# Kernel tuning notes

Hardware: AMD Instinct MI355X
Metric: run time of the kernel (lower is better)

Reference implementation:

```python
import jax, jax.numpy as jnp
import numpy as np

# db4 (Daubechies-4) lowpass decomposition filter, L = 8 taps
DB4 = np.array([0.23037781330885523, 0.7148465705525415, 0.6308807679295904,
                -0.027983769416983849, -0.18703481171888114, 0.030841381835986965,
                0.032883011666982945, -0.010597401784997278], dtype=np.float32)


def setup_inputs() -> dict:
    key = jax.random.key(0)
    x = jax.random.normal(key, (4, 256, 256, 256), dtype=jnp.float32)
    h = jnp.asarray(DB4)
    return {"x": x, "h": h}


def _corr_valid(u, f):
    # u: [..., T], f: [L]; cross-correlation with VALID padding (== tf.nn.conv1d)
    L = f.shape[0]
    B = int(np.prod(u.shape[:-1]))
    out = jax.lax.conv_general_dilated(
        u.reshape(B, 1, u.shape[-1]), f.reshape(1, 1, L),
        window_strides=(1,), padding='VALID',
        dimension_numbers=('NCW', 'OIW', 'NCW'))
    return out.reshape(u.shape[:-1] + (out.shape[-1],))


def _recon_axis(s, w, h0, h1, axis):
    # s, w: scale / wavelet coefficient halves, same shape; recon along `axis`
    L = h0.shape[0]
    P = (L - 2) // 2 + 1  # number of periodic-wrap samples (= L//2 for even L)
    x = jnp.stack([s, w])                      # [2, ...]
    x = jnp.moveaxis(x, axis + 1, -1)          # bring recon axis to last
    N = x.shape[-1]
    # periodic extension (cyclic gather of last P) then drop first -> len N+P-1
    x = jnp.concatenate([x[..., N - P:], x], axis=-1)[..., 1:]
    # zero-interleaved upsample: [0, x0, 0, x1, ...], then one trailing zero -> len 2N+L-1
    up = jnp.stack([jnp.zeros_like(x), x], axis=-1).reshape(x.shape[:-1] + (-1,))
    up = jnp.pad(up, [(0, 0)] * (up.ndim - 1) + [(0, 1)])
    y = _corr_valid(up[0], h0) + _corr_valid(up[1], h1)  # [..., 2N]
    return jnp.moveaxis(y, -1, axis)


def reference(x, h):
    h0 = h[::-1]                                        # reversed lowpass
    sign = jnp.where(jnp.arange(h.shape[0]) % 2 == 0, -1.0, 1.0).astype(h.dtype)
    h1 = sign * h                                       # QMF highpass (double reverse cancels)
    out = x
    for axis in range(1, x.ndim):
        s, w = jnp.split(out, 2, axis=axis)
        out = _recon_axis(s, w, h0, h1, axis)
    return out
```

## Files before the change

### kernel.cpp

```cpp
#include <hip/hip_runtime.h>


typedef float f32x2 __attribute__((ext_vector_type(2)));

#define FILT_DECL(h)                                          \
  const float a0 = h[6], a1 = h[4], a2 = h[2], a3 = h[0];     \
  const float b0 = h[7], b1 = h[5], b2 = h[3], b3 = h[1];     \
  const float c0 = h[1], c1 = h[3], c2 = h[5], c3 = h[7];     \
  const float d0 = -h[0], d1 = -h[2], d2 = -h[4], d3 = -h[6];

#define Y0(s0,s1,s2,s3,w0,w1,w2,w3)                                        \
  fmaf(w3, c3, fmaf(w2, c2, fmaf(w1, c1, fmaf(w0, c0,                      \
  fmaf(s3, a3, fmaf(s2, a2, fmaf(s1, a1, s0 * a0)))))))
#define Y1(s0,s1,s2,s3,w0,w1,w2,w3)                                        \
  fmaf(w3, d3, fmaf(w2, d2, fmaf(w1, d1, fmaf(w0, d0,                      \
  fmaf(s3, b3, fmaf(s2, b2, fmaf(s1, b1, s0 * b0)))))))

#define PKFMA(s, k, acc) __builtin_elementwise_fma((f32x2){(s),(s)}, (k), (acc))

__device__ __forceinline__ void gload_lds4(const float* g, float* l) {
  auto gp = reinterpret_cast<const __attribute__((address_space(1))) int*>(
      reinterpret_cast<uintptr_t>(g));
  auto lp = reinterpret_cast<__attribute__((address_space(3))) int*>(
      reinterpret_cast<uintptr_t>(l));
  __builtin_amdgcn_global_load_lds(gp, lp, 4, 0, 0);
}

__global__ __launch_bounds__(256) void wav_axis1_s(const float* __restrict__ in,
                                                   float* __restrict__ tmp,
                                                   const float* __restrict__ h) {
  const int inner = blockIdx.x * 256 + threadIdx.x;
  const int m0 = blockIdx.y * 64;
  const size_t base = (size_t)blockIdx.z * (256u * 65536u) + (unsigned)inner;
  const float* __restrict__ ps = in + base;
  const float* __restrict__ pw = in + base + (size_t)128 * 65536;
  float* __restrict__ po = tmp + base;
  FILT_DECL(h)
  float s0 = __builtin_nontemporal_load(&ps[(size_t)((m0 - 3) & 127) * 65536]);
  float s1 = __builtin_nontemporal_load(&ps[(size_t)((m0 - 2) & 127) * 65536]);
  float s2 = __builtin_nontemporal_load(&ps[(size_t)((m0 - 1) & 127) * 65536]);
  float w0 = __builtin_nontemporal_load(&pw[(size_t)((m0 - 3) & 127) * 65536]);
  float w1 = __builtin_nontemporal_load(&pw[(size_t)((m0 - 2) & 127) * 65536]);
  float w2 = __builtin_nontemporal_load(&pw[(size_t)((m0 - 1) & 127) * 65536]);
  for (int m = m0; m < m0 + 64; ++m) {
    const float s3 = __builtin_nontemporal_load(&ps[(size_t)m * 65536]);
    const float w3 = __builtin_nontemporal_load(&pw[(size_t)m * 65536]);
    po[(size_t)(2 * m) * 65536] = Y0(s0, s1, s2, s3, w0, w1, w2, w3);
    po[(size_t)(2 * m + 1) * 65536] = Y1(s0, s1, s2, s3, w0, w1, w2, w3);
    s0 = s1; s1 = s2; s2 = s3;
    w0 = w1; w1 = w2; w2 = w3;
  }
}

#define LSTR 264
__global__ __launch_bounds__(256, 7) void wav_t23s(const float* __restrict__ tmp,
                                                   float* __restrict__ out,
                                                   const float* __restrict__ hg) {
  __shared__ __align__(16) float lb[22 * LSTR];
  const int t = threadIdx.x;
  const int d2t = blockIdx.x;
  const size_t slice = blockIdx.y;
  const float* __restrict__ src = tmp + slice * 65536;
  FILT_DECL(hg)
  const f32x2 AB0 = {a0, b0}, AB1 = {a1, b1}, AB2 = {a2, b2}, AB3 = {a3, b3};
  const f32x2 CD0 = {c0, d0}, CD1 = {c1, d1}, CD2 = {c2, d2}, CD3 = {c3, d3};
  const int mb2 = 8 * d2t - 3;

  {
    const int phys = t + ((t < 128) ? 3 : 7);
#pragma unroll
    for (int k = 0; k < 11; ++k) {
      const int g2 = (mb2 + k) & 127;
      gload_lds4(src + (g2 << 8) + t, &lb[k * LSTR + phys]);
    }
#pragma unroll
    for (int k = 0; k < 11; ++k) {
      const int g2 = 128 + ((mb2 + k) & 127);
      gload_lds4(src + (g2 << 8) + t, &lb[(11 + k) * LSTR + phys]);
    }
  }
  __syncthreads();

  {
    const int pj = t + ((t < 128) ? 3 : 7);
    float S[11], W[11];
#pragma unroll
    for (int i = 0; i < 11; ++i) S[i] = lb[i * LSTR + pj];
#pragma unroll
    for (int i = 0; i < 11; ++i) W[i] = lb[(11 + i) * LSTR + pj];
    const int hcol = (t >= 125 && t < 128) ? (t - 125)
                   : ((t >= 253) ? (t - 121) : -1);
#pragma unroll
    for (int q = 0; q < 8; ++q) {
      f32x2 acc = (f32x2){S[q], S[q]} * AB0;
      acc = PKFMA(S[q+1], AB1, acc);
      acc = PKFMA(S[q+2], AB2, acc);
      acc = PKFMA(S[q+3], AB3, acc);
      acc = PKFMA(W[q],   CD0, acc);
      acc = PKFMA(W[q+1], CD1, acc);
      acc = PKFMA(W[q+2], CD2, acc);
      acc = PKFMA(W[q+3], CD3, acc);
      lb[q * LSTR + pj] = acc.x;
      lb[(11 + q) * LSTR + pj] = acc.y;
      if (hcol >= 0) {
        lb[q * LSTR + hcol] = acc.x;
        lb[(11 + q) * LSTR + hcol] = acc.y;
      }
    }
  }
  __syncthreads();

  const int r = t >> 4, m0 = (t & 15) * 8;
  const int prow = ((r & 1) ? (11 + (r >> 1)) : (r >> 1)) * LSTR;
  float S[11], W[11];
  {
    const float4 sa = *reinterpret_cast<const float4*>(&lb[prow + m0]);
    const float4 sb = *reinterpret_cast<const float4*>(&lb[prow + m0 + 4]);
    const float2 sc = *reinterpret_cast<const float2*>(&lb[prow + m0 + 8]);
    S[0]=sa.x; S[1]=sa.y; S[2]=sa.z; S[3]=sa.w;
    S[4]=sb.x; S[5]=sb.y; S[6]=sb.z; S[7]=sb.w;
    S[8]=sc.x; S[9]=sc.y; S[10]=lb[prow + m0 + 10];
    const float4 wa = *reinterpret_cast<const float4*>(&lb[prow + 132 + m0]);
    const float4 wb = *reinterpret_cast<const float4*>(&lb[prow + 132 + m0 + 4]);
    const float2 wc = *reinterpret_cast<const float2*>(&lb[prow + 132 + m0 + 8]);
    W[0]=wa.x; W[1]=wa.y; W[2]=wa.z; W[3]=wa.w;
    W[4]=wb.x; W[5]=wb.y; W[6]=wb.z; W[7]=wb.w;
    W[8]=wc.x; W[9]=wc.y; W[10]=lb[prow + 132 + m0 + 10];
  }
  float* __restrict__ dst = out + slice * 65536
      + (size_t)(16 * d2t + r) * 256 + 16 * (t & 15);
#pragma unroll
  for (int g = 0; g < 4; ++g) {
    f32x2 eA = (f32x2){S[2*g], S[2*g]} * AB0;
    eA = PKFMA(S[2*g+1], AB1, eA);
    eA = PKFMA(S[2*g+2], AB2, eA);
    eA = PKFMA(S[2*g+3], AB3, eA);
    eA = PKFMA(W[2*g],   CD0, eA);
    eA = PKFMA(W[2*g+1], CD1, eA);
    eA = PKFMA(W[2*g+2], CD2, eA);
    eA = PKFMA(W[2*g+3], CD3, eA);
    f32x2 eB = (f32x2){S[2*g+1], S[2*g+1]} * AB0;
    eB = PKFMA(S[2*g+2], AB1, eB);
    eB = PKFMA(S[2*g+3], AB2, eB);
    eB = PKFMA(S[2*g+4], AB3, eB);
    eB = PKFMA(W[2*g+1], CD0, eB);
    eB = PKFMA(W[2*g+2], CD1, eB);
    eB = PKFMA(W[2*g+3], CD2, eB);
    eB = PKFMA(W[2*g+4], CD3, eB);
    *reinterpret_cast<float4*>(dst + 4 * g) = make_float4(eA.x, eA.y, eB.x, eB.y);
  }
}

__global__ __launch_bounds__(256) void wav_axis1(const float* __restrict__ in,
                                                 float* __restrict__ out,
                                                 const float* __restrict__ h) {
  const int inner = blockIdx.x * 256 + threadIdx.x;
  const int m0 = blockIdx.y * 64;
  const size_t base = (size_t)blockIdx.z * (256u * 65536u) + (unsigned)inner;
  const float* __restrict__ ps = in + base;
  const float* __restrict__ pw = in + base + (size_t)128 * 65536;
  float* __restrict__ po = out + base;
  FILT_DECL(h)
  float s0 = ps[(size_t)((m0 - 3) & 127) * 65536];
  float s1 = ps[(size_t)((m0 - 2) & 127) * 65536];
  float s2 = ps[(size_t)((m0 - 1) & 127) * 65536];
  float w0 = pw[(size_t)((m0 - 3) & 127) * 65536];
  float w1 = pw[(size_t)((m0 - 2) & 127) * 65536];
  float w2 = pw[(size_t)((m0 - 1) & 127) * 65536];
  for (int m = m0; m < m0 + 64; ++m) {
    const float s3 = ps[(size_t)m * 65536];
    const float w3 = pw[(size_t)m * 65536];
    po[(size_t)(2 * m) * 65536] = Y0(s0, s1, s2, s3, w0, w1, w2, w3);
    po[(size_t)(2 * m + 1) * 65536] = Y1(s0, s1, s2, s3, w0, w1, w2, w3);
    s0 = s1; s1 = s2; s2 = s3;
    w0 = w1; w1 = w2; w2 = w3;
  }
}

__global__ __launch_bounds__(256) void wav_axis2(float* __restrict__ buf,
                                                 const float* __restrict__ h) {
  __shared__ float tile[256][32];
  const int t = threadIdx.x;
  const int c = t & 31;
  const int g = t >> 5;
  const size_t slice = (size_t)(blockIdx.x >> 3);
  const int col0 = (blockIdx.x & 7) * 32;
  float* __restrict__ p = buf + slice * 65536 + col0;
#pragma unroll
  for (int i = 0; i < 32; ++i) {
    const int rr = i * 8 + g;
    tile[rr][c] = p[rr * 256 + c];
  }
  __syncthreads();
  FILT_DECL(h)
  const int m0 = g * 16;
  float s0 = tile[(m0 - 3) & 127][c];
  float s1 = tile[(m0 - 2) & 127][c];
  float s2 = tile[(m0 - 1) & 127][c];
  float w0 = tile[128 + ((m0 - 3) & 127)][c];
  float w1 = tile[128 + ((m0 - 2) & 127)][c];
  float w2 = tile[128 + ((m0 - 1) & 127)][c];
#pragma unroll
  for (int m = m0; m < m0 + 16; ++m) {
    const float s3 = tile[m][c];
    const float w3 = tile[128 + m][c];
    p[(2 * m) * 256 + c] = Y0(s0, s1, s2, s3, w0, w1, w2, w3);
    p[(2 * m + 1) * 256 + c] = Y1(s0, s1, s2, s3, w0, w1, w2, w3);
    s0 = s1; s1 = s2; s2 = s3;
    w0 = w1; w1 = w2; w2 = w3;
  }
}

__global__ __launch_bounds__(256) void wav_axis3(float* __restrict__ buf,
                                                 const float* __restrict__ h) {
  __shared__ float tile[512];
  const int t = threadIdx.x;
  float* __restrict__ p = buf + (size_t)blockIdx.x * 512;
  tile[t] = p[t];
  tile[256 + t] = p[256 + t];
  __syncthreads();
  FILT_DECL(h)
  const int rr = t >> 7;
  const int m = t & 127;
  const float* __restrict__ line = tile + rr * 256;
  const float s0 = line[(m - 3) & 127];
  const float s1 = line[(m - 2) & 127];
  const float s2 = line[(m - 1) & 127];
  const float s3 = line[m];
  const float w0 = line[128 + ((m - 3) & 127)];
  const float w1 = line[128 + ((m - 2) & 127)];
  const float w2 = line[128 + ((m - 1) & 127)];
  const float w3 = line[128 + m];
  float2 y;
  y.x = Y0(s0, s1, s2, s3, w0, w1, w2, w3);
  y.y = Y1(s0, s1, s2, s3, w0, w1, w2, w3);
  *reinterpret_cast<float2*>(p + rr * 256 + 2 * m) = y;
}

extern "C" void kernel_launch(void* const* d_in, const int* in_sizes, int n_in,
                              void* d_out, int out_size, void* d_ws, size_t ws_size,
                              hipStream_t stream) {
  const float* x = (const float*)d_in[0];
  const float* h = (const float*)d_in[1];
  float* out = (float*)d_out;
  const size_t need = (size_t)4 * 256 * 256 * 256 * 4;

  if (ws_size >= need) {
    float* tmp = (float*)d_ws;
    wav_axis1_s<<<dim3(256, 2, 4), 256, 0, stream>>>(x, tmp, h);
    wav_t23s<<<dim3(16, 1024), 256, 0, stream>>>(tmp, out, h);
  } else {
    wav_axis1<<<dim3(256, 2, 4), 256, 0, stream>>>(x, out, h);
    wav_axis2<<<dim3(8192), 256, 0, stream>>>(out, h);
    wav_axis3<<<dim3(131072), 256, 0, stream>>>(out, h);
  }
}
```

Measured before the change: 220.6 us.

## Make second-stage kernel persistent per slice with double-buffered LDS prefetch

The fused axis-2/3 kernel now launches one block per 256x256 slice instead of one block per 16-row tile. Each block walks all 16 tiles in a loop, and the async global-to-LDS loads for the next tile go into a second LDS buffer while the current tile is computed. The aim is to hide global load latency behind compute and cut per-block launch and setup cost. In exchange the grid shrinks to 1024 blocks, per-block LDS usage doubles and the occupancy hint is dropped, so fewer waves may be resident per CU to hide memory latency.

```diff
diff --git a/kernel.cpp b/kernel.cpp
--- a/kernel.cpp
+++ b/kernel.cpp
@@ -53,101 +53,113 @@
 }
 
 #define LSTR 264
-__global__ __launch_bounds__(256, 7) void wav_t23s(const float* __restrict__ tmp,
-                                                   float* __restrict__ out,
-                                                   const float* __restrict__ hg) {
-  __shared__ __align__(16) float lb[22 * LSTR];
+__global__ __launch_bounds__(256) void wav_t23p(const float* __restrict__ tmp,
+                                                float* __restrict__ out,
+                                                const float* __restrict__ hg) {
+  __shared__ __align__(16) float lb[2][22 * LSTR];
   const int t = threadIdx.x;
-  const int d2t = blockIdx.x;
-  const size_t slice = blockIdx.y;
+  const size_t slice = blockIdx.x;
   const float* __restrict__ src = tmp + slice * 65536;
+  float* __restrict__ dstb = out + slice * 65536 + 16 * (t & 15);
   FILT_DECL(hg)
   const f32x2 AB0 = {a0, b0}, AB1 = {a1, b1}, AB2 = {a2, b2}, AB3 = {a3, b3};
   const f32x2 CD0 = {c0, d0}, CD1 = {c1, d1}, CD2 = {c2, d2}, CD3 = {c3, d3};
-  const int mb2 = 8 * d2t - 3;
-
-  {
-    const int phys = t + ((t < 128) ? 3 : 7);
-#pragma unroll
-    for (int k = 0; k < 11; ++k) {
-      const int g2 = (mb2 + k) & 127;
-      gload_lds4(src + (g2 << 8) + t, &lb[k * LSTR + phys]);
-    }
-#pragma unroll
-    for (int k = 0; k < 11; ++k) {
-      const int g2 = 128 + ((mb2 + k) & 127);
-      gload_lds4(src + (g2 << 8) + t, &lb[(11 + k) * LSTR + phys]);
-    }
-  }
-  __syncthreads();
-
-  {
-    const int pj = t + ((t < 128) ? 3 : 7);
-    float S[11], W[11];
-#pragma unroll
-    for (int i = 0; i < 11; ++i) S[i] = lb[i * LSTR + pj];
-#pragma unroll
-    for (int i = 0; i < 11; ++i) W[i] = lb[(11 + i) * LSTR + pj];
-    const int hcol = (t >= 125 && t < 128) ? (t - 125)
-                   : ((t >= 253) ? (t - 121) : -1);
-#pragma unroll
-    for (int q = 0; q < 8; ++q) {
-      f32x2 acc = (f32x2){S[q], S[q]} * AB0;
-      acc = PKFMA(S[q+1], AB1, acc);
-      acc = PKFMA(S[q+2], AB2, acc);
-      acc = PKFMA(S[q+3], AB3, acc);
-      acc = PKFMA(W[q],   CD0, acc);
-      acc = PKFMA(W[q+1], CD1, acc);
-      acc = PKFMA(W[q+2], CD2, acc);
-      acc = PKFMA(W[q+3], CD3, acc);
-      lb[q * LSTR + pj] = acc.x;
-      lb[(11 + q) * LSTR + pj] = acc.y;
-      if (hcol >= 0) {
-        lb[q * LSTR + hcol] = acc.x;
-        lb[(11 + q) * LSTR + hcol] = acc.y;
-      }
-    }
-  }
-  __syncthreads();
-
+  const int phys = t + ((t < 128) ? 3 : 7);
+  const int hcol = (t >= 125 && t < 128) ? (t - 125)
+                 : ((t >= 253) ? (t - 121) : -1);
   const int r = t >> 4, m0 = (t & 15) * 8;
   const int prow = ((r & 1) ? (11 + (r >> 1)) : (r >> 1)) * LSTR;
-  float S[11], W[11];
+
   {
-    const float4 sa = *reinterpret_cast<const float4*>(&lb[prow + m0]);
-    const float4 sb = *reinterpret_cast<const float4*>(&lb[prow + m0 + 4]);
-    const float2 sc = *reinterpret_cast<const float2*>(&lb[prow + m0 + 8]);
-    S[0]=sa.x; S[1]=sa.y; S[2]=sa.z; S[3]=sa.w;
-    S[4]=sb.x; S[5]=sb.y; S[6]=sb.z; S[7]=sb.w;
-    S[8]=sc.x; S[9]=sc.y; S[10]=lb[prow + m0 + 10];
-    const float4 wa = *reinterpret_cast<const float4*>(&lb[prow + 132 + m0]);
-    const float4 wb = *reinterpret_cast<const float4*>(&lb[prow + 132 + m0 + 4]);
-    const float2 wc = *reinterpret_cast<const float2*>(&lb[prow + 132 + m0 + 8]);
-    W[0]=wa.x; W[1]=wa.y; W[2]=wa.z; W[3]=wa.w;
-    W[4]=wb.x; W[5]=wb.y; W[6]=wb.z; W[7]=wb.w;
-    W[8]=wc.x; W[9]=wc.y; W[10]=lb[prow + 132 + m0 + 10];
-  }
-  float* __restrict__ dst = out + slice * 65536
-      + (size_t)(16 * d2t + r) * 256 + 16 * (t & 15);
-#pragma unroll
-  for (int g = 0; g < 4; ++g) {
-    f32x2 eA = (f32x2){S[2*g], S[2*g]} * AB0;
-    eA = PKFMA(S[2*g+1], AB1, eA);
-    eA = PKFMA(S[2*g+2], AB2, eA);
-    eA = PKFMA(S[2*g+3], AB3, eA);
-    eA = PKFMA(W[2*g],   CD0, eA);
-    eA = PKFMA(W[2*g+1], CD1, eA);
-    eA = PKFMA(W[2*g+2], CD2, eA);
-    eA = PKFMA(W[2*g+3], CD3, eA);
-    f32x2 eB = (f32x2){S[2*g+1], S[2*g+1]} * AB0;
-    eB = PKFMA(S[2*g+2], AB1, eB);
-    eB = PKFMA(S[2*g+3], AB2, eB);
-    eB = PKFMA(S[2*g+4], AB3, eB);
-    eB = PKFMA(W[2*g+1], CD0, eB);
-    eB = PKFMA(W[2*g+2], CD1, eB);
-    eB = PKFMA(W[2*g+3], CD2, eB);
-    eB = PKFMA(W[2*g+4], CD3, eB);
-    *reinterpret_cast<float4*>(dst + 4 * g) = make_float4(eA.x, eA.y, eB.x, eB.y);
+    const int mb2 = -3;
+#pragma unroll
+    for (int kk = 0; kk < 11; ++kk) {
+      const int g2 = (mb2 + kk) & 127;
+      gload_lds4(src + (g2 << 8) + t, &lb[0][kk * LSTR + phys]);
+      gload_lds4(src + ((128 + g2) << 8) + t, &lb[0][(11 + kk) * LSTR + phys]);
+    }
+  }
+
+  for (int d2t = 0; d2t < 16; ++d2t) {
+    const int cur = d2t & 1;
+    __syncthreads();
+
+    if (d2t < 15) {
+      const int mb2 = 8 * (d2t + 1) - 3;
+      float* bb = lb[cur ^ 1];
+#pragma unroll
+      for (int kk = 0; kk < 11; ++kk) {
+        const int g2 = (mb2 + kk) & 127;
+        gload_lds4(src + (g2 << 8) + t, &bb[kk * LSTR + phys]);
+        gload_lds4(src + ((128 + g2) << 8) + t, &bb[(11 + kk) * LSTR + phys]);
+      }
+    }
+
+    float* __restrict__ lbc = lb[cur];
+
+    {
+      float S[11], W[11];
+#pragma unroll
+      for (int i = 0; i < 11; ++i) S[i] = lbc[i * LSTR + phys];
+#pragma unroll
+      for (int i = 0; i < 11; ++i) W[i] = lbc[(11 + i) * LSTR + phys];
+#pragma unroll
+      for (int q = 0; q < 8; ++q) {
+        f32x2 acc = (f32x2){S[q], S[q]} * AB0;
+        acc = PKFMA(S[q+1], AB1, acc);
+        acc = PKFMA(S[q+2], AB2, acc);
+        acc = PKFMA(S[q+3], AB3, acc);
+        acc = PKFMA(W[q],   CD0, acc);
+        acc = PKFMA(W[q+1], CD1, acc);
+        acc = PKFMA(W[q+2], CD2, acc);
+        acc = PKFMA(W[q+3], CD3, acc);
+        lbc[q * LSTR + phys] = acc.x;
+        lbc[(11 + q) * LSTR + phys] = acc.y;
+        if (hcol >= 0) {
+          lbc[q * LSTR + hcol] = acc.x;
+          lbc[(11 + q) * LSTR + hcol] = acc.y;
+        }
+      }
+    }
+
+    asm volatile("s_waitcnt lgkmcnt(0)\n\ts_barrier" ::: "memory");
+
+    float S[11], W[11];
+    {
+      const float4 sa = *reinterpret_cast<const float4*>(&lbc[prow + m0]);
+      const float4 sb = *reinterpret_cast<const float4*>(&lbc[prow + m0 + 4]);
+      const float2 sc = *reinterpret_cast<const float2*>(&lbc[prow + m0 + 8]);
+      S[0]=sa.x; S[1]=sa.y; S[2]=sa.z; S[3]=sa.w;
+      S[4]=sb.x; S[5]=sb.y; S[6]=sb.z; S[7]=sb.w;
+      S[8]=sc.x; S[9]=sc.y; S[10]=lbc[prow + m0 + 10];
+      const float4 wa = *reinterpret_cast<const float4*>(&lbc[prow + 132 + m0]);
+      const float4 wb = *reinterpret_cast<const float4*>(&lbc[prow + 132 + m0 + 4]);
+      const float2 wc = *reinterpret_cast<const float2*>(&lbc[prow + 132 + m0 + 8]);
+      W[0]=wa.x; W[1]=wa.y; W[2]=wa.z; W[3]=wa.w;
+      W[4]=wb.x; W[5]=wb.y; W[6]=wb.z; W[7]=wb.w;
+      W[8]=wc.x; W[9]=wc.y; W[10]=lbc[prow + 132 + m0 + 10];
+    }
+    float* __restrict__ dst = dstb + (size_t)(16 * d2t + r) * 256;
+#pragma unroll
+    for (int g = 0; g < 4; ++g) {
+      f32x2 eA = (f32x2){S[2*g], S[2*g]} * AB0;
+      eA = PKFMA(S[2*g+1], AB1, eA);
+      eA = PKFMA(S[2*g+2], AB2, eA);
+      eA = PKFMA(S[2*g+3], AB3, eA);
+      eA = PKFMA(W[2*g],   CD0, eA);
+      eA = PKFMA(W[2*g+1], CD1, eA);
+      eA = PKFMA(W[2*g+2], CD2, eA);
+      eA = PKFMA(W[2*g+3], CD3, eA);
+      f32x2 eB = (f32x2){S[2*g+1], S[2*g+1]} * AB0;
+      eB = PKFMA(S[2*g+2], AB1, eB);
+      eB = PKFMA(S[2*g+3], AB2, eB);
+      eB = PKFMA(S[2*g+4], AB3, eB);
+      eB = PKFMA(W[2*g+1], CD0, eB);
+      eB = PKFMA(W[2*g+2], CD1, eB);
+      eB = PKFMA(W[2*g+3], CD2, eB);
+      eB = PKFMA(W[2*g+4], CD3, eB);
+      *reinterpret_cast<float4*>(dst + 4 * g) = make_float4(eA.x, eA.y, eB.x, eB.y);
+    }
   }
 }
 
@@ -248,7 +260,7 @@
   if (ws_size >= need) {
     float* tmp = (float*)d_ws;
     wav_axis1_s<<<dim3(256, 2, 4), 256, 0, stream>>>(x, tmp, h);
-    wav_t23s<<<dim3(16, 1024), 256, 0, stream>>>(tmp, out, h);
+    wav_t23p<<<dim3(1024), 256, 0, stream>>>(tmp, out, h);
   } else {
     wav_axis1<<<dim3(256, 2, 4), 256, 0, stream>>>(x, out, h);
     wav_axis2<<<dim3(8192), 256, 0, stream>>>(out, h);
```

Measured after the change: 246.3 us. 11.7% more time.

## Make axis-2/3 kernel persistent over eight tiles with register prefetch of next tile

Applied to the files above, without the earlier changes.

Each block of the fused axis-2/3 reconstruction kernel now handles eight consecutive row tiles of a slice instead of one, which cuts the grid from 16K blocks to 2048. While the current tile is computed, the next tile's 22 input rows are loaded from global memory into registers and then written into LDS after a barrier. The aim is to overlap global loads with compute and amortize block launch and prologue cost. In exchange, register pressure rises (occupancy hint drops from 7 to 4), direct-to-LDS loads are replaced by register staging, and extra barriers are added per tile.

```diff
diff --git a/kernel.cpp b/kernel.cpp
--- a/kernel.cpp
+++ b/kernel.cpp
@@ -53,101 +53,119 @@
 }
 
 #define LSTR 264
-__global__ __launch_bounds__(256, 7) void wav_t23s(const float* __restrict__ tmp,
+__global__ __launch_bounds__(256, 4) void wav_t23f(const float* __restrict__ tmp,
                                                    float* __restrict__ out,
                                                    const float* __restrict__ hg) {
   __shared__ __align__(16) float lb[22 * LSTR];
   const int t = threadIdx.x;
-  const int d2t = blockIdx.x;
-  const size_t slice = blockIdx.y;
+  const size_t slice = blockIdx.x >> 1;
+  const int t0 = (blockIdx.x & 1) * 8;
   const float* __restrict__ src = tmp + slice * 65536;
+  float* __restrict__ outs = out + slice * 65536;
   FILT_DECL(hg)
   const f32x2 AB0 = {a0, b0}, AB1 = {a1, b1}, AB2 = {a2, b2}, AB3 = {a3, b3};
   const f32x2 CD0 = {c0, d0}, CD1 = {c1, d1}, CD2 = {c2, d2}, CD3 = {c3, d3};
-  const int mb2 = 8 * d2t - 3;
-
-  {
-    const int phys = t + ((t < 128) ? 3 : 7);
-#pragma unroll
-    for (int k = 0; k < 11; ++k) {
-      const int g2 = (mb2 + k) & 127;
-      gload_lds4(src + (g2 << 8) + t, &lb[k * LSTR + phys]);
-    }
-#pragma unroll
-    for (int k = 0; k < 11; ++k) {
-      const int g2 = 128 + ((mb2 + k) & 127);
-      gload_lds4(src + (g2 << 8) + t, &lb[(11 + k) * LSTR + phys]);
-    }
-  }
-  __syncthreads();
-
-  {
-    const int pj = t + ((t < 128) ? 3 : 7);
-    float S[11], W[11];
-#pragma unroll
-    for (int i = 0; i < 11; ++i) S[i] = lb[i * LSTR + pj];
-#pragma unroll
-    for (int i = 0; i < 11; ++i) W[i] = lb[(11 + i) * LSTR + pj];
-    const int hcol = (t >= 125 && t < 128) ? (t - 125)
-                   : ((t >= 253) ? (t - 121) : -1);
-#pragma unroll
-    for (int q = 0; q < 8; ++q) {
-      f32x2 acc = (f32x2){S[q], S[q]} * AB0;
-      acc = PKFMA(S[q+1], AB1, acc);
-      acc = PKFMA(S[q+2], AB2, acc);
-      acc = PKFMA(S[q+3], AB3, acc);
-      acc = PKFMA(W[q],   CD0, acc);
-      acc = PKFMA(W[q+1], CD1, acc);
-      acc = PKFMA(W[q+2], CD2, acc);
-      acc = PKFMA(W[q+3], CD3, acc);
-      lb[q * LSTR + pj] = acc.x;
-      lb[(11 + q) * LSTR + pj] = acc.y;
-      if (hcol >= 0) {
-        lb[q * LSTR + hcol] = acc.x;
-        lb[(11 + q) * LSTR + hcol] = acc.y;
-      }
-    }
-  }
-  __syncthreads();
-
+  const int phys = t + ((t < 128) ? 3 : 7);
+  const int hcol = (t >= 125 && t < 128) ? (t - 125)
+                 : ((t >= 253) ? (t - 121) : -1);
   const int r = t >> 4, m0 = (t & 15) * 8;
   const int prow = ((r & 1) ? (11 + (r >> 1)) : (r >> 1)) * LSTR;
-  float S[11], W[11];
+
   {
-    const float4 sa = *reinterpret_cast<const float4*>(&lb[prow + m0]);
-    const float4 sb = *reinterpret_cast<const float4*>(&lb[prow + m0 + 4]);
-    const float2 sc = *reinterpret_cast<const float2*>(&lb[prow + m0 + 8]);
-    S[0]=sa.x; S[1]=sa.y; S[2]=sa.z; S[3]=sa.w;
-    S[4]=sb.x; S[5]=sb.y; S[6]=sb.z; S[7]=sb.w;
-    S[8]=sc.x; S[9]=sc.y; S[10]=lb[prow + m0 + 10];
-    const float4 wa = *reinterpret_cast<const float4*>(&lb[prow + 132 + m0]);
-    const float4 wb = *reinterpret_cast<const float4*>(&lb[prow + 132 + m0 + 4]);
-    const float2 wc = *reinterpret_cast<const float2*>(&lb[prow + 132 + m0 + 8]);
-    W[0]=wa.x; W[1]=wa.y; W[2]=wa.z; W[3]=wa.w;
-    W[4]=wb.x; W[5]=wb.y; W[6]=wb.z; W[7]=wb.w;
-    W[8]=wc.x; W[9]=wc.y; W[10]=lb[prow + 132 + m0 + 10];
-  }
-  float* __restrict__ dst = out + slice * 65536
-      + (size_t)(16 * d2t + r) * 256 + 16 * (t & 15);
-#pragma unroll
-  for (int g = 0; g < 4; ++g) {
-    f32x2 eA = (f32x2){S[2*g], S[2*g]} * AB0;
-    eA = PKFMA(S[2*g+1], AB1, eA);
-    eA = PKFMA(S[2*g+2], AB2, eA);
-    eA = PKFMA(S[2*g+3], AB3, eA);
-    eA = PKFMA(W[2*g],   CD0, eA);
-    eA = PKFMA(W[2*g+1], CD1, eA);
-    eA = PKFMA(W[2*g+2], CD2, eA);
-    eA = PKFMA(W[2*g+3], CD3, eA);
-    f32x2 eB = (f32x2){S[2*g+1], S[2*g+1]} * AB0;
-    eB = PKFMA(S[2*g+2], AB1, eB);
-    eB = PKFMA(S[2*g+3], AB2, eB);
-    eB = PKFMA(S[2*g+4], AB3, eB);
-    eB = PKFMA(W[2*g+1], CD0, eB);
-    eB = PKFMA(W[2*g+2], CD1, eB);
-    eB = PKFMA(W[2*g+3], CD2, eB);
-    eB = PKFMA(W[2*g+4], CD3, eB);
-    *reinterpret_cast<float4*>(dst + 4 * g) = make_float4(eA.x, eA.y, eB.x, eB.y);
+    const int mb2 = 8 * t0 - 3;
+#pragma unroll
+    for (int kk = 0; kk < 11; ++kk) {
+      const int g2 = (mb2 + kk) & 127;
+      gload_lds4(src + (g2 << 8) + t, &lb[kk * LSTR + phys]);
+      gload_lds4(src + ((128 + g2) << 8) + t, &lb[(11 + kk) * LSTR + phys]);
+    }
+  }
+  __syncthreads();
+
+  for (int k = 0; k < 8; ++k) {
+    float nx[22];
+    if (k < 7) {
+      const int mb2 = 8 * (t0 + k + 1) - 3;
+#pragma unroll
+      for (int kk = 0; kk < 11; ++kk) {
+        const int g2 = (mb2 + kk) & 127;
+        nx[kk]      = src[(g2 << 8) + t];
+        nx[11 + kk] = src[((128 + g2) << 8) + t];
+      }
+    }
+
+    {
+      float S[11], W[11];
+#pragma unroll
+      for (int i = 0; i < 11; ++i) S[i] = lb[i * LSTR + phys];
+#pragma unroll
+      for (int i = 0; i < 11; ++i) W[i] = lb[(11 + i) * LSTR + phys];
+#pragma unroll
+      for (int q = 0; q < 8; ++q) {
+        f32x2 acc = (f32x2){S[q], S[q]} * AB0;
+        acc = PKFMA(S[q+1], AB1, acc);
+        acc = PKFMA(S[q+2], AB2, acc);
+        acc = PKFMA(S[q+3], AB3, acc);
+        acc = PKFMA(W[q],   CD0, acc);
+        acc = PKFMA(W[q+1], CD1, acc);
+        acc = PKFMA(W[q+2], CD2, acc);
+        acc = PKFMA(W[q+3], CD3, acc);
+        lb[q * LSTR + phys] = acc.x;
+        lb[(11 + q) * LSTR + phys] = acc.y;
+        if (hcol >= 0) {
+          lb[q * LSTR + hcol] = acc.x;
+          lb[(11 + q) * LSTR + hcol] = acc.y;
+        }
+      }
+    }
+    asm volatile("s_waitcnt lgkmcnt(0)\n\ts_barrier" ::: "memory");
+
+    float S[11], W[11];
+    {
+      const float4 sa = *reinterpret_cast<const float4*>(&lb[prow + m0]);
+      const float4 sb = *reinterpret_cast<const float4*>(&lb[prow + m0 + 4]);
+      const float2 sc = *reinterpret_cast<const float2*>(&lb[prow + m0 + 8]);
+      S[0]=sa.x; S[1]=sa.y; S[2]=sa.z; S[3]=sa.w;
+      S[4]=sb.x; S[5]=sb.y; S[6]=sb.z; S[7]=sb.w;
+      S[8]=sc.x; S[9]=sc.y; S[10]=lb[prow + m0 + 10];
+      const float4 wa = *reinterpret_cast<const float4*>(&lb[prow + 132 + m0]);
+      const float4 wb = *reinterpret_cast<const float4*>(&lb[prow + 132 + m0 + 4]);
+      const float2 wc = *reinterpret_cast<const float2*>(&lb[prow + 132 + m0 + 8]);
+      W[0]=wa.x; W[1]=wa.y; W[2]=wa.z; W[3]=wa.w;
+      W[4]=wb.x; W[5]=wb.y; W[6]=wb.z; W[7]=wb.w;
+      W[8]=wc.x; W[9]=wc.y; W[10]=lb[prow + 132 + m0 + 10];
+    }
+    float* __restrict__ dst = outs + (size_t)(16 * (t0 + k) + r) * 256 + 16 * (t & 15);
+#pragma unroll
+    for (int g = 0; g < 4; ++g) {
+      f32x2 eA = (f32x2){S[2*g], S[2*g]} * AB0;
+      eA = PKFMA(S[2*g+1], AB1, eA);
+      eA = PKFMA(S[2*g+2], AB2, eA);
+      eA = PKFMA(S[2*g+3], AB3, eA);
+      eA = PKFMA(W[2*g],   CD0, eA);
+      eA = PKFMA(W[2*g+1], CD1, eA);
+      eA = PKFMA(W[2*g+2], CD2, eA);
+      eA = PKFMA(W[2*g+3], CD3, eA);
+      f32x2 eB = (f32x2){S[2*g+1], S[2*g+1]} * AB0;
+      eB = PKFMA(S[2*g+2], AB1, eB);
+      eB = PKFMA(S[2*g+3], AB2, eB);
+      eB = PKFMA(S[2*g+4], AB3, eB);
+      eB = PKFMA(W[2*g+1], CD0, eB);
+      eB = PKFMA(W[2*g+2], CD1, eB);
+      eB = PKFMA(W[2*g+3], CD2, eB);
+      eB = PKFMA(W[2*g+4], CD3, eB);
+      *reinterpret_cast<float4*>(dst + 4 * g) = make_float4(eA.x, eA.y, eB.x, eB.y);
+    }
+
+    if (k < 7) {
+      asm volatile("s_barrier" ::: "memory");
+#pragma unroll
+      for (int kk = 0; kk < 11; ++kk) {
+        lb[kk * LSTR + phys]        = nx[kk];
+        lb[(11 + kk) * LSTR + phys] = nx[11 + kk];
+      }
+      asm volatile("s_waitcnt lgkmcnt(0)\n\ts_barrier" ::: "memory");
+    }
   }
 }
 
@@ -248,7 +266,7 @@
   if (ws_size >= need) {
     float* tmp = (float*)d_ws;
     wav_axis1_s<<<dim3(256, 2, 4), 256, 0, stream>>>(x, tmp, h);
-    wav_t23s<<<dim3(16, 1024), 256, 0, stream>>>(tmp, out, h);
+    wav_t23f<<<dim3(2048), 256, 0, stream>>>(tmp, out, h);
   } else {
     wav_axis1<<<dim3(256, 2, 4), 256, 0, stream>>>(x, out, h);
     wav_axis2<<<dim3(8192), 256, 0, stream>>>(out, h);
```

New measurement: 230.2 us. 4.3% more time.
